# Optimization experiments

Measured on AMD Instinct MI355X. Metric: run time of the kernel, lower is better.

The kernel has to match this reference:

```python
import jax, jax.numpy as jnp
import numpy as np

N = 4096
D = 1024          # latent_vector_size
H, KD, VD = 16, 64, 64
MHK = H * KD      # 1024
MHV = H * VD      # 1024
HID = D // 2      # 512
EPS = 1e-5


def _layernorm(v, g, b):
    mu = jnp.mean(v, axis=-1, keepdims=True)
    var = jnp.mean(jnp.square(v - mu), axis=-1, keepdims=True)
    return (v - mu) * jax.lax.rsqrt(var + EPS) * g + b


def setup_inputs() -> dict:
    key = jax.random.key(0)
    ks = jax.random.split(key, 12)
    s = lambda fan_in: 1.0 / np.sqrt(fan_in)
    return {
        "x": jax.random.normal(ks[0], (N, D), dtype=jnp.float32),
        "w_qkv": jax.random.uniform(ks[1], (D, H * (2 * KD + VD)), jnp.float32, -s(D), s(D)),
        "b_qkv": jax.random.uniform(ks[2], (H * (2 * KD + VD),), jnp.float32, -s(D), s(D)),
        "w_msa": jax.random.uniform(ks[3], (MHV, D), jnp.float32, -s(MHV), s(MHV)),
        "b_msa": jax.random.uniform(ks[4], (D,), jnp.float32, -s(MHV), s(MHV)),
        "ln_g": jnp.ones((D,), jnp.float32),
        "ln_b": jnp.zeros((D,), jnp.float32),
        "w_h1": jax.random.uniform(ks[5], (D, HID), jnp.float32, -s(D), s(D)),
        "b_h1": jax.random.uniform(ks[6], (HID,), jnp.float32, -s(D), s(D)),
        "w_h2": jax.random.uniform(ks[7], (HID, D), jnp.float32, -s(HID), s(HID)),
        "b_h2": jax.random.uniform(ks[8], (D,), jnp.float32, -s(HID), s(HID)),
    }


def reference(x, w_qkv, b_qkv, w_msa, b_msa, ln_g, ln_b, w_h1, b_h1, w_h2, b_h2):
    # --- attention block (note: heads are never split; one big [N,N] softmax) ---
    ln1 = _layernorm(x, ln_g, ln_b)                       # [N, D]
    qkv = ln1 @ w_qkv + b_qkv                             # [N, 3*MHK]
    q, k, v = qkv[:, :MHK], qkv[:, MHK:2 * MHK], qkv[:, 2 * MHK:]
    scores = (q @ k.T) / jnp.sqrt(jnp.float32(KD))        # [N, N]
    attn = jax.nn.softmax(scores, axis=-1)
    mha = (attn @ v) @ w_msa + b_msa                      # [N, D]
    enc1 = x + mha
    # --- MLP block (shared layernorm params; softmax output, residual) ---
    ln2 = _layernorm(enc1, ln_g, ln_b)
    h1 = jax.nn.gelu(ln2 @ w_h1 + b_h1, approximate=False)  # [N, HID]
    h2 = jax.nn.gelu(h1 @ w_h2 + b_h2, approximate=False)   # [N, D]
    out = jax.nn.softmax(h2, axis=-1)                        # nn.Softmax() -> dim=1 for 2D
    return enc1 + out
```

## Files before the change

### kernel.cpp

```cpp
#include <hip/hip_runtime.h>
#include <stdint.h>

#define DEV __device__ __forceinline__

typedef unsigned short u16;
typedef __attribute__((ext_vector_type(8))) unsigned short u16x8;
typedef __attribute__((ext_vector_type(4))) unsigned short u16x4;
typedef __attribute__((ext_vector_type(4))) float f32x4;

DEV float bf2f(u16 u) { return __uint_as_float(((unsigned)u) << 16); }
DEV u16 f2bf(float f) {
  unsigned u = __float_as_uint(f);
  u += 0x7FFFu + ((u >> 16) & 1u);
  return (u16)(u >> 16);
}
DEV float gelu_exact(float v) { return 0.5f * v * (1.0f + erff(v * 0.70710678118654752f)); }

#define BARF asm volatile("s_barrier" ::: "memory")

__global__ __launch_bounds__(256) void transpose4_f32_bf16(
    const float* __restrict__ wqkv, u16* __restrict__ wqkvT,
    const float* __restrict__ wmsa, u16* __restrict__ wmsaT,
    const float* __restrict__ wh1, u16* __restrict__ wh1T,
    const float* __restrict__ wh2, u16* __restrict__ wh2T) {
  __shared__ float t[32][33];
  const int id = blockIdx.x;
  const float* in; u16* out; int rows, cols, bx, by;
  if (id < 3072)      { in = wqkv; out = wqkvT; rows = 1024; cols = 3072; bx = id % 96;          by = id / 96; }
  else if (id < 4096) { in = wmsa; out = wmsaT; rows = 1024; cols = 1024; bx = (id - 3072) % 32; by = (id - 3072) / 32; }
  else if (id < 4608) { in = wh1;  out = wh1T;  rows = 1024; cols = 512;  bx = (id - 4096) % 16; by = (id - 4096) / 16; }
  else                { in = wh2;  out = wh2T;  rows = 512;  cols = 1024; bx = (id - 4608) % 32; by = (id - 4608) / 32; }
  const int tx = threadIdx.x, ty = threadIdx.y;
  const int c0 = bx * 32, r0 = by * 32;
#pragma unroll
  for (int i = 0; i < 32; i += 8) t[ty + i][tx] = in[(size_t)(r0 + ty + i) * cols + c0 + tx];
  __syncthreads();
#pragma unroll
  for (int i = 0; i < 32; i += 8)
    out[(size_t)(c0 + ty + i) * rows + r0 + tx] = f2bf(t[tx][ty + i]);
}

__global__ __launch_bounds__(256) void transpose_bf16(
    const u16* __restrict__ in, int ldin, u16* __restrict__ out, int ldout) {
  __shared__ u16 t[32][33];
  const int tx = threadIdx.x, ty = threadIdx.y;
  const int c0 = blockIdx.x * 32, r0 = blockIdx.y * 32;
#pragma unroll
  for (int i = 0; i < 32; i += 8) t[ty + i][tx] = in[(size_t)(r0 + ty + i) * ldin + c0 + tx];
  __syncthreads();
#pragma unroll
  for (int i = 0; i < 32; i += 8)
    out[(size_t)(c0 + ty + i) * ldout + r0 + tx] = t[tx][ty + i];
}

__global__ __launch_bounds__(256) void layernorm_bf16(
    const float* __restrict__ in, const float* __restrict__ g,
    const float* __restrict__ b, u16* __restrict__ out) {
  const int tid = threadIdx.x;
  const int lane = tid & 63, wid = tid >> 6;
  const size_t base = (size_t)blockIdx.x * 1024;
  const float4 v = ((const float4*)(in + base))[tid];
  float s = v.x + v.y + v.z + v.w;
  float ss = v.x * v.x + v.y * v.y + v.z * v.z + v.w * v.w;
#pragma unroll
  for (int off = 32; off > 0; off >>= 1) {
    s += __shfl_down(s, off);
    ss += __shfl_down(ss, off);
  }
  __shared__ float red[8];
  if (lane == 0) { red[wid] = s; red[4 + wid] = ss; }
  __syncthreads();
  s = red[0] + red[1] + red[2] + red[3];
  ss = red[4] + red[5] + red[6] + red[7];
  const float mu = s * (1.0f / 1024.0f);
  const float inv = rsqrtf(ss * (1.0f / 1024.0f) - mu * mu + 1e-5f);
  const float4 gv = ((const float4*)g)[tid];
  const float4 bv = ((const float4*)b)[tid];
  u16x4 o;
  o.x = f2bf((v.x - mu) * inv * gv.x + bv.x);
  o.y = f2bf((v.y - mu) * inv * gv.y + bv.y);
  o.z = f2bf((v.z - mu) * inv * gv.z + bv.z);
  o.w = f2bf((v.w - mu) * inv * gv.w + bv.w);
  *(u16x4*)(out + base + tid * 4) = o;
}

__global__ __launch_bounds__(256) void softmax4096(u16* __restrict__ p) {
  const int tid = threadIdx.x;
  const int lane = tid & 63, wid = tid >> 6;
  u16* row = p + (size_t)blockIdx.x * 4096;
  u16x8 r0 = ((u16x8*)row)[tid * 2];
  u16x8 r1 = ((u16x8*)row)[tid * 2 + 1];
  float v[16];
#pragma unroll
  for (int i = 0; i < 8; ++i) { v[i] = bf2f(r0[i]); v[8 + i] = bf2f(r1[i]); }
  float mx = v[0];
#pragma unroll
  for (int i = 1; i < 16; ++i) mx = fmaxf(mx, v[i]);
#pragma unroll
  for (int off = 32; off > 0; off >>= 1) mx = fmaxf(mx, __shfl_down(mx, off));
  __shared__ float red[8];
  if (lane == 0) red[wid] = mx;
  __syncthreads();
  mx = fmaxf(fmaxf(red[0], red[1]), fmaxf(red[2], red[3]));
  float sum = 0.0f;
#pragma unroll
  for (int i = 0; i < 16; ++i) { v[i] = __expf(v[i] - mx); sum += v[i]; }
#pragma unroll
  for (int off = 32; off > 0; off >>= 1) sum += __shfl_down(sum, off);
  if (lane == 0) red[4 + wid] = sum;
  __syncthreads();
  sum = red[4] + red[5] + red[6] + red[7];
  const float inv = 1.0f / sum;
  u16x8 o0, o1;
#pragma unroll
  for (int i = 0; i < 8; ++i) { o0[i] = f2bf(v[i] * inv); o1[i] = f2bf(v[8 + i] * inv); }
  ((u16x8*)row)[tid * 2] = o0;
  ((u16x8*)row)[tid * 2 + 1] = o1;
}

__global__ __launch_bounds__(256) void final_softmax_add(
    const float* __restrict__ h2, const float* __restrict__ enc1, float* __restrict__ out) {
  const int tid = threadIdx.x;
  const int lane = tid & 63, wid = tid >> 6;
  const size_t base = (size_t)blockIdx.x * 1024;
  float4 v = ((const float4*)(h2 + base))[tid];
  float mx = fmaxf(fmaxf(v.x, v.y), fmaxf(v.z, v.w));
#pragma unroll
  for (int off = 32; off > 0; off >>= 1) mx = fmaxf(mx, __shfl_down(mx, off));
  __shared__ float red[8];
  if (lane == 0) red[wid] = mx;
  __syncthreads();
  mx = fmaxf(fmaxf(red[0], red[1]), fmaxf(red[2], red[3]));
  v.x = __expf(v.x - mx); v.y = __expf(v.y - mx);
  v.z = __expf(v.z - mx); v.w = __expf(v.w - mx);
  float sum = v.x + v.y + v.z + v.w;
#pragma unroll
  for (int off = 32; off > 0; off >>= 1) sum += __shfl_down(sum, off);
  if (lane == 0) red[4 + wid] = sum;
  __syncthreads();
  sum = red[4] + red[5] + red[6] + red[7];
  const float inv = 1.0f / sum;
  const float4 e = ((const float4*)(enc1 + base))[tid];
  float4 o;
  o.x = e.x + v.x * inv; o.y = e.y + v.y * inv;
  o.z = e.z + v.z * inv; o.w = e.w + v.w * inv;
  ((float4*)(out + base))[tid] = o;
}

__global__ __launch_bounds__(256) void reduce_partials(
    const u16* __restrict__ P, u16* __restrict__ out) {
  const size_t i = ((size_t)blockIdx.x * 256 + threadIdx.x) * 8;
  const size_t S = 4096ull * 1024ull;
  u16x8 p0 = *(const u16x8*)(P + i);
  u16x8 p1 = *(const u16x8*)(P + S + i);
  u16x8 p2 = *(const u16x8*)(P + 2 * S + i);
  u16x8 p3 = *(const u16x8*)(P + 3 * S + i);
  u16x8 o;
#pragma unroll
  for (int j = 0; j < 8; ++j)
    o[j] = f2bf(bf2f(p0[j]) + bf2f(p1[j]) + bf2f(p2[j]) + bf2f(p3[j]));
  *(u16x8*)(out + i) = o;
}

template <int EPI>
__global__ __launch_bounds__(512, 2) void gemm256(
    const u16* __restrict__ A, int lda, const u16* __restrict__ Bt, int ldb,
    u16* __restrict__ C, int ldc, const float* __restrict__ bias, float scale,
    int K, int nsplit, size_t sliceStride) {
  __shared__ alignas(16) u16 As[2][16384];
  __shared__ alignas(16) u16 Bs[2][16384];
  const int tid = threadIdx.x;
  const int wid = tid >> 6;
  const int lane = tid & 63;
  const int wr = wid >> 2, wc = wid & 3;

  const int gx = gridDim.x;
  const int nwg = gx * gridDim.y;
  int wg = blockIdx.y * gx + blockIdx.x;
  wg = (wg & 7) * (nwg >> 3) + (wg >> 3);
  const int by = wg / gx;
  const int bxk = wg % gx;
  const int ks = bxk % nsplit;
  const int bx = bxk / nsplit;
  const int m0 = by * 256, n0 = bx * 256;
  A += (size_t)ks * K;
  Bt += (size_t)ks * K;
  C += (size_t)ks * sliceStride;

  const u16* Apan = A + (size_t)m0 * lda;
  const u16* Bpan = Bt + (size_t)n0 * ldb;

  const int sgk = ((lane & 7) ^ ((lane >> 3) & 7)) * 8;
  const int hi4 = lane >> 4;
  const int kgo0 = ((0 * 4 + hi4) ^ (lane & 7)) * 8;
  const int kgo1 = ((1 * 4 + hi4) ^ (lane & 7)) * 8;
  const int arowo = (wr * 128 + (lane & 15)) * 64;
  const int browo = (wc * 64 + (lane & 15)) * 64;

  f32x4 acc[8][4];
#pragma unroll
  for (int m = 0; m < 8; ++m)
#pragma unroll
    for (int n = 0; n < 4; ++n) { f32x4 z = {0.f, 0.f, 0.f, 0.f}; acc[m][n] = z; }

  u16x8 a[2][2], b[4][2];

#define ST_HALF(dst, pan, ld, t, h)                                              \
  {                                                                              \
    _Pragma("unroll") for (int j = 0; j < 2; ++j) {                              \
      const int chunk = (tid >> 6) * 2 + j;                                      \
      const int row = (h)*128 + chunk * 8 + (lane >> 3);                         \
      const u16* gsrc = (pan) + (size_t)row * (ld) + (t)*64 + sgk;               \
      __builtin_amdgcn_global_load_lds(                                          \
          (const __attribute__((address_space(1))) void*)gsrc,                   \
          (__attribute__((address_space(3))) void*)((dst) + (h)*8192 +           \
                                                    chunk * 512 + lane * 8),     \
          16, 0, 0);                                                             \
    }                                                                            \
  }

#define LOADB(S)                                                                 \
  _Pragma("unroll") for (int n = 0; n < 4; ++n) {                                \
    b[n][0] = *(const u16x8*)&Bs[S][browo + n * 1024 + kgo0];                    \
    b[n][1] = *(const u16x8*)&Bs[S][browo + n * 1024 + kgo1];                    \
  }

#define LOADA(S, Q)                                                              \
  _Pragma("unroll") for (int mi = 0; mi < 2; ++mi) {                             \
    a[mi][0] = *(const u16x8*)&As[S][arowo + (2 * (Q) + mi) * 1024 + kgo0];      \
    a[mi][1] = *(const u16x8*)&As[S][arowo + (2 * (Q) + mi) * 1024 + kgo1];      \
  }

#define MMQ(Q)                                                                   \
  BARF;                                                                          \
  __builtin_amdgcn_s_setprio(1);                                                 \
  _Pragma("unroll") for (int mi = 0; mi < 2; ++mi)                               \
      _Pragma("unroll") for (int n = 0; n < 4; ++n)                              \
          _Pragma("unroll") for (int kk = 0; kk < 2; ++kk)                       \
              asm("v_mfma_f32_16x16x32_bf16 %0, %1, %2, %0"                      \
                  : "+v"(acc[2 * ((Q) & 3) + mi][n])                             \
                  : "v"(a[mi][kk]), "v"(b[n][kk]));                              \
  __builtin_amdgcn_s_setprio(0);

#define VMW asm volatile("s_waitcnt vmcnt(4)" ::: "memory");

  const int NT = K >> 6;
  const int NI = NT >> 1;

  ST_HALF(&Bs[0][0], Bpan, ldb, 0, 0);
  ST_HALF(&Bs[0][0], Bpan, ldb, 0, 1);
  ST_HALF(&As[0][0], Apan, lda, 0, 0);
  ST_HALF(&As[0][0], Apan, lda, 0, 1);
  ST_HALF(&Bs[1][0], Bpan, ldb, 1, 0);
  ST_HALF(&Bs[1][0], Bpan, ldb, 1, 1);
  VMW;
  BARF;

  for (int it = 0; it < NI; ++it) {
    const int t0 = 2 * it, t1 = t0 + 1;
    const int tS0 = (t0 + 2 < NT) ? t0 + 2 : NT - 1;
    const int tS1 = (t1 + 2 < NT) ? t1 + 2 : NT - 1;
    LOADB(0); LOADA(0, 0);
    ST_HALF(&As[1][0], Apan, lda, t1, 0);
    ST_HALF(&As[1][0], Apan, lda, t1, 1);
    MMQ(0); BARF;
    LOADA(0, 1);
    ST_HALF(&Bs[0][0], Bpan, ldb, tS0, 0);
    MMQ(1); BARF;
    LOADA(0, 2);
    ST_HALF(&Bs[0][0], Bpan, ldb, tS0, 1);
    MMQ(2); BARF;
    LOADA(0, 3);
    MMQ(3); VMW; BARF;
    LOADB(1); LOADA(1, 0);
    ST_HALF(&As[0][0], Apan, lda, tS0, 0);
    ST_HALF(&As[0][0], Apan, lda, tS0, 1);
    MMQ(4); BARF;
    LOADA(1, 1);
    ST_HALF(&Bs[1][0], Bpan, ldb, tS1, 0);
    MMQ(5); BARF;
    LOADA(1, 2);
    ST_HALF(&Bs[1][0], Bpan, ldb, tS1, 1);
    MMQ(6); BARF;
    LOADA(1, 3);
    MMQ(7); VMW; BARF;
  }
  asm volatile("s_waitcnt vmcnt(0)" ::: "memory");
  BARF;

  const int crow0 = m0 + wr * 128 + hi4 * 4;
  const int ccol0 = n0 + wc * 64 + (lane & 15);
#pragma unroll
  for (int m = 0; m < 8; ++m) {
#pragma unroll
    for (int n = 0; n < 4; ++n) {
      const int col = ccol0 + n * 16;
      float bia = 0.0f;
      if (EPI == 1) bia = bias[col];
#pragma unroll
      for (int r = 0; r < 4; ++r) {
        const int row = crow0 + m * 16 + r;
        float v = acc[m][n][r];
        if (EPI == 0) v *= scale;
        if (EPI == 1) v += bia;
        C[(size_t)row * ldc + col] = f2bf(v);
      }
    }
  }
#undef ST_HALF
#undef LOADB
#undef LOADA
#undef MMQ
#undef VMW
}

template <int EPI>
__global__ __launch_bounds__(256) void gemm_bt(
    const u16* __restrict__ A, int lda, const u16* __restrict__ Bt, int ldb,
    void* __restrict__ Cv, int ldc, const float* __restrict__ bias,
    const float* __restrict__ xres, int ldx, float scale, int K) {
  __shared__ alignas(16) u16 As[3][128 * 32];
  __shared__ alignas(16) u16 Bs[3][128 * 32];
  const int tid = threadIdx.x;
  const int wid = tid >> 6;
  const int lane = tid & 63;

  const int gx = gridDim.x;
  const int nwg = gridDim.x * gridDim.y;
  int wg = blockIdx.y * gx + blockIdx.x;
  wg = (wg & 7) * (nwg >> 3) + (wg >> 3);
  const int m0 = (wg / gx) * 128;
  const int n0 = (wg % gx) * 128;
  const int wr = wid >> 1, wc = wid & 1;

  const int srow = lane >> 2;
  const int sseg = (((lane & 3) ^ ((lane >> 3) & 3))) * 8;

  f32x4 acc[4][4];
#pragma unroll
  for (int m = 0; m < 4; ++m)
#pragma unroll
    for (int n = 0; n < 4; ++n) { f32x4 z = {0.f, 0.f, 0.f, 0.f}; acc[m][n] = z; }

  const int arow = wr * 64 + (lane & 15);
  const int brow = wc * 64 + (lane & 15);
  const int koff = (((lane >> 4) ^ ((lane >> 1) & 3))) * 8;

  const int NT = K >> 5;

  auto STAGE = [&](int kt, int buf) {
    const int k0 = kt * 32;
#pragma unroll
    for (int i = 0; i < 2; ++i) {
      const int r = i * 64 + wid * 16;
      const u16* ga = A + (size_t)(m0 + r + srow) * lda + k0 + sseg;
      const u16* gb = Bt + (size_t)(n0 + r + srow) * ldb + k0 + sseg;
      __builtin_amdgcn_global_load_lds((const __attribute__((address_space(1))) void*)ga,
                                       (__attribute__((address_space(3))) void*)&As[buf][r * 32], 16, 0, 0);
      __builtin_amdgcn_global_load_lds((const __attribute__((address_space(1))) void*)gb,
                                       (__attribute__((address_space(3))) void*)&Bs[buf][r * 32], 16, 0, 0);
    }
  };

  STAGE(0, 0);
  STAGE(1, 1);
  asm volatile("s_waitcnt vmcnt(4)" ::: "memory");
  BARF;

  int cur = 0;
  for (int t = 0; t < NT; ++t) {
    const int kt = (t + 2 < NT) ? (t + 2) : (NT - 1);
    STAGE(kt, (cur + 2) % 3);

    u16x8 a[4], b[4];
#pragma unroll
    for (int m = 0; m < 4; ++m) a[m] = *(const u16x8*)&As[cur][(arow + m * 16) * 32 + koff];
#pragma unroll
    for (int n = 0; n < 4; ++n) b[n] = *(const u16x8*)&Bs[cur][(brow + n * 16) * 32 + koff];
#pragma unroll
    for (int m = 0; m < 4; ++m)
#pragma unroll
      for (int n = 0; n < 4; ++n)
        asm("v_mfma_f32_16x16x32_bf16 %0, %1, %2, %0" : "+v"(acc[m][n]) : "v"(a[m]), "v"(b[n]));

    asm volatile("s_waitcnt vmcnt(4)" ::: "memory");
    BARF;
    cur = (cur + 1) % 3;
  }

  const int crow0 = m0 + wr * 64 + ((lane >> 4) << 2);
  const int ccol0 = n0 + wc * 64 + (lane & 15);
#pragma unroll
  for (int m = 0; m < 4; ++m) {
#pragma unroll
    for (int n = 0; n < 4; ++n) {
      const int col = ccol0 + n * 16;
      float bia = 0.0f;
      if (EPI == 3 || EPI == 4 || EPI == 5) bia = bias[col];
#pragma unroll
      for (int r = 0; r < 4; ++r) {
        const int row = crow0 + m * 16 + r;
        const float v = acc[m][n][r];
        if (EPI == 3) {
          ((float*)Cv)[(size_t)row * ldc + col] = v + bia + xres[(size_t)row * ldx + col];
        } else if (EPI == 4) {
          ((u16*)Cv)[(size_t)row * ldc + col] = f2bf(gelu_exact(v + bia));
        } else {
          ((float*)Cv)[(size_t)row * ldc + col] = gelu_exact(v + bia);
        }
      }
    }
  }
}

extern "C" void kernel_launch(void* const* d_in, const int* in_sizes, int n_in,
                              void* d_out, int out_size, void* d_ws, size_t ws_size,
                              hipStream_t stream) {
  const float* x     = (const float*)d_in[0];
  const float* w_qkv = (const float*)d_in[1];
  const float* b_qkv = (const float*)d_in[2];
  const float* w_msa = (const float*)d_in[3];
  const float* b_msa = (const float*)d_in[4];
  const float* ln_g  = (const float*)d_in[5];
  const float* ln_b  = (const float*)d_in[6];
  const float* w_h1  = (const float*)d_in[7];
  const float* b_h1  = (const float*)d_in[8];
  const float* w_h2  = (const float*)d_in[9];
  const float* b_h2  = (const float*)d_in[10];

  char* w = (char*)d_ws;
  u16*   qkv   = (u16*)(w + 0);
  u16*   sc    = (u16*)(w + 25165824);
  u16*   lnb   = (u16*)(w + 58720256);
  u16*   av    = (u16*)(w + 67108864);
  u16*   vT    = (u16*)(w + 75497472);
  float* enc1  = (float*)(w + 83886080);
  u16*   part  = (u16*)(w + 83886080);
  u16*   h1    = (u16*)(w + 100663296);
  float* h2    = (float*)(w + 104857600);
  u16*   wqkvT = (u16*)(w + 121634816);
  u16*   wmsaT = (u16*)(w + 127926272);
  u16*   wh1T  = (u16*)(w + 130023424);
  u16*   wh2T  = (u16*)(w + 131072000);
  (void)in_sizes; (void)n_in; (void)out_size; (void)ws_size;

  dim3 tb(32, 8);
  transpose4_f32_bf16<<<5120, tb, 0, stream>>>(w_qkv, wqkvT, w_msa, wmsaT,
                                               w_h1, wh1T, w_h2, wh2T);

  layernorm_bf16<<<4096, 256, 0, stream>>>(x, ln_g, ln_b, lnb);
  gemm256<1><<<dim3(12, 16), 512, 0, stream>>>(lnb, 1024, wqkvT, 1024, qkv, 3072,
                                               b_qkv, 1.0f, 1024, 1, 0);
  transpose_bf16<<<dim3(32, 128), tb, 0, stream>>>(qkv + 2048, 3072, vT, 4096);
  gemm256<0><<<dim3(16, 16), 512, 0, stream>>>(qkv, 3072, qkv + 1024, 3072, sc, 4096,
                                               nullptr, 0.125f, 1024, 1, 0);
  softmax4096<<<4096, 256, 0, stream>>>(sc);
  gemm256<2><<<dim3(16, 16), 512, 0, stream>>>(sc, 4096, vT, 4096, part, 1024,
                                               nullptr, 1.0f, 1024, 4, 4096ull * 1024ull);
  reduce_partials<<<2048, 256, 0, stream>>>(part, av);
  gemm_bt<3><<<dim3(8, 32), 256, 0, stream>>>(av, 1024, wmsaT, 1024, enc1, 1024,
                                              b_msa, x, 1024, 1.0f, 1024);
  layernorm_bf16<<<4096, 256, 0, stream>>>(enc1, ln_g, ln_b, lnb);
  gemm_bt<4><<<dim3(4, 32), 256, 0, stream>>>(lnb, 1024, wh1T, 1024, h1, 512,
                                              b_h1, nullptr, 0, 1.0f, 1024);
  gemm_bt<5><<<dim3(8, 32), 256, 0, stream>>>(h1, 512, wh2T, 512, h2, 1024,
                                              b_h2, nullptr, 0, 1.0f, 512);
  final_softmax_add<<<4096, 256, 0, stream>>>(h2, enc1, (float*)d_out);
}
```

Before: 233.7 us.

## Restructure GEMM main loop with double A register buffers and fewer barriers

Reorganises the inner K loop of the MFMA GEMM so each 64-wide K tile is processed in two halves. Two register buffers for A fragments let two quarter-tiles of MFMAs issue back-to-back, which cuts the per-tile barrier count from about five to two. Global-to-LDS prefetches are grouped after a single barrier and overlap the second half of the MFMAs. The trade-offs are higher VGPR pressure and less interleaving of loads with compute, which could hurt occupancy or latency hiding.

Measured after the change: 230.3 us. About the same (-1.5%).

```diff
diff --git a/kernel.cpp b/kernel.cpp
--- a/kernel.cpp
+++ b/kernel.cpp
@@ -203,7 +203,7 @@
 #pragma unroll
     for (int n = 0; n < 4; ++n) { f32x4 z = {0.f, 0.f, 0.f, 0.f}; acc[m][n] = z; }
 
-  u16x8 a[2][2], b[4][2];
+  u16x8 a0[2][2], a1[2][2], b[4][2];
 
 #define ST_HALF(dst, pan, ld, t, h)                                              \
   {                                                                              \
@@ -225,22 +225,19 @@
     b[n][1] = *(const u16x8*)&Bs[S][browo + n * 1024 + kgo1];                    \
   }
 
-#define LOADA(S, Q)                                                              \
+#define LOADA(S, Q, DST)                                                         \
   _Pragma("unroll") for (int mi = 0; mi < 2; ++mi) {                             \
-    a[mi][0] = *(const u16x8*)&As[S][arowo + (2 * (Q) + mi) * 1024 + kgo0];      \
-    a[mi][1] = *(const u16x8*)&As[S][arowo + (2 * (Q) + mi) * 1024 + kgo1];      \
-  }
-
-#define MMQ(Q)                                                                   \
-  BARF;                                                                          \
-  __builtin_amdgcn_s_setprio(1);                                                 \
+    DST[mi][0] = *(const u16x8*)&As[S][arowo + (2 * (Q) + mi) * 1024 + kgo0];    \
+    DST[mi][1] = *(const u16x8*)&As[S][arowo + (2 * (Q) + mi) * 1024 + kgo1];    \
+  }
+
+#define MFMAQ(SRC, Q)                                                            \
   _Pragma("unroll") for (int mi = 0; mi < 2; ++mi)                               \
       _Pragma("unroll") for (int n = 0; n < 4; ++n)                              \
           _Pragma("unroll") for (int kk = 0; kk < 2; ++kk)                       \
               asm("v_mfma_f32_16x16x32_bf16 %0, %1, %2, %0"                      \
-                  : "+v"(acc[2 * ((Q) & 3) + mi][n])                             \
-                  : "v"(a[mi][kk]), "v"(b[n][kk]));                              \
-  __builtin_amdgcn_s_setprio(0);
+                  : "+v"(acc[2 * (Q) + mi][n])                                   \
+                  : "v"(SRC[mi][kk]), "v"(b[n][kk]));
 
 #define VMW asm volatile("s_waitcnt vmcnt(4)" ::: "memory");
 
@@ -257,33 +254,43 @@
   BARF;
 
   for (int it = 0; it < NI; ++it) {
-    const int t0 = 2 * it, t1 = t0 + 1;
-    const int tS0 = (t0 + 2 < NT) ? t0 + 2 : NT - 1;
-    const int tS1 = (t1 + 2 < NT) ? t1 + 2 : NT - 1;
-    LOADB(0); LOADA(0, 0);
+    const int t1 = 2 * it + 1;
+    const int tS0 = (2 * it + 2 < NT) ? 2 * it + 2 : NT - 1;
+    const int tS1 = (2 * it + 3 < NT) ? 2 * it + 3 : NT - 1;
+
+    LOADB(0);
+    LOADA(0, 0, a0); LOADA(0, 1, a1);
+    __builtin_amdgcn_s_setprio(1);
+    MFMAQ(a0, 0); MFMAQ(a1, 1);
+    __builtin_amdgcn_s_setprio(0);
+    LOADA(0, 2, a0); LOADA(0, 3, a1);
+    BARF;
     ST_HALF(&As[1][0], Apan, lda, t1, 0);
     ST_HALF(&As[1][0], Apan, lda, t1, 1);
-    MMQ(0); BARF;
-    LOADA(0, 1);
     ST_HALF(&Bs[0][0], Bpan, ldb, tS0, 0);
-    MMQ(1); BARF;
-    LOADA(0, 2);
     ST_HALF(&Bs[0][0], Bpan, ldb, tS0, 1);
-    MMQ(2); BARF;
-    LOADA(0, 3);
-    MMQ(3); VMW; BARF;
-    LOADB(1); LOADA(1, 0);
+    __builtin_amdgcn_s_setprio(1);
+    MFMAQ(a0, 2); MFMAQ(a1, 3);
+    __builtin_amdgcn_s_setprio(0);
+    VMW;
+    BARF;
+
+    LOADB(1);
+    LOADA(1, 0, a0); LOADA(1, 1, a1);
+    __builtin_amdgcn_s_setprio(1);
+    MFMAQ(a0, 0); MFMAQ(a1, 1);
+    __builtin_amdgcn_s_setprio(0);
+    LOADA(1, 2, a0); LOADA(1, 3, a1);
+    BARF;
     ST_HALF(&As[0][0], Apan, lda, tS0, 0);
     ST_HALF(&As[0][0], Apan, lda, tS0, 1);
-    MMQ(4); BARF;
-    LOADA(1, 1);
     ST_HALF(&Bs[1][0], Bpan, ldb, tS1, 0);
-    MMQ(5); BARF;
-    LOADA(1, 2);
     ST_HALF(&Bs[1][0], Bpan, ldb, tS1, 1);
-    MMQ(6); BARF;
-    LOADA(1, 3);
-    MMQ(7); VMW; BARF;
+    __builtin_amdgcn_s_setprio(1);
+    MFMAQ(a0, 2); MFMAQ(a1, 3);
+    __builtin_amdgcn_s_setprio(0);
+    VMW;
+    BARF;
   }
   asm volatile("s_waitcnt vmcnt(0)" ::: "memory");
   BARF;
@@ -310,7 +317,7 @@
 #undef ST_HALF
 #undef LOADB
 #undef LOADA
-#undef MMQ
+#undef MFMAQ
 #undef VMW
 }
 
```

## Run output projection through split-K gemm256 with fused bias-residual reduction

Applied to the files above, without the earlier changes.

The attention output projection now uses the large 256-tile GEMM with 4-way split-K into bf16 partials. A new reduce kernel sums them and adds bias and the residual in fp32. The GEMM inner loops switch from inline-asm MFMA to the compiler builtin, with an explicit LDS wait and reordered stage loads. enc1 is moved to alias the qkv buffer. The new path adds extra partial-buffer traffic and bf16 rounding of partials in exchange for better tile utilization.

Result: slower. 241.3 us (+3.2%).

```diff
diff --git a/kernel.cpp b/kernel.cpp
--- a/kernel.cpp
+++ b/kernel.cpp
@@ -5,6 +5,7 @@
 
 typedef unsigned short u16;
 typedef __attribute__((ext_vector_type(8))) unsigned short u16x8;
+typedef __attribute__((ext_vector_type(8))) short s16x8;
 typedef __attribute__((ext_vector_type(4))) unsigned short u16x4;
 typedef __attribute__((ext_vector_type(4))) float f32x4;
 
@@ -162,6 +163,33 @@
   *(u16x8*)(out + i) = o;
 }
 
+__global__ __launch_bounds__(256) void reduce4_bias_res(
+    const u16* __restrict__ P, const float* __restrict__ bias,
+    const float* __restrict__ x, float* __restrict__ out) {
+  const size_t i = ((size_t)blockIdx.x * 256 + threadIdx.x) * 8;
+  const size_t S = 4096ull * 1024ull;
+  u16x8 p0 = *(const u16x8*)(P + i);
+  u16x8 p1 = *(const u16x8*)(P + S + i);
+  u16x8 p2 = *(const u16x8*)(P + 2 * S + i);
+  u16x8 p3 = *(const u16x8*)(P + 3 * S + i);
+  const int col = (int)(i & 1023);
+  const float4 b0 = *(const float4*)(bias + col);
+  const float4 b1 = *(const float4*)(bias + col + 4);
+  const float4 x0 = *(const float4*)(x + i);
+  const float4 x1 = *(const float4*)(x + i + 4);
+  float r[8];
+#pragma unroll
+  for (int j = 0; j < 8; ++j)
+    r[j] = bf2f(p0[j]) + bf2f(p1[j]) + bf2f(p2[j]) + bf2f(p3[j]);
+  float4 o0, o1;
+  o0.x = r[0] + b0.x + x0.x; o0.y = r[1] + b0.y + x0.y;
+  o0.z = r[2] + b0.z + x0.z; o0.w = r[3] + b0.w + x0.w;
+  o1.x = r[4] + b1.x + x1.x; o1.y = r[5] + b1.y + x1.y;
+  o1.z = r[6] + b1.z + x1.z; o1.w = r[7] + b1.w + x1.w;
+  *(float4*)(out + i) = o0;
+  *(float4*)(out + i + 4) = o1;
+}
+
 template <int EPI>
 __global__ __launch_bounds__(512, 2) void gemm256(
     const u16* __restrict__ A, int lda, const u16* __restrict__ Bt, int ldb,
@@ -170,8 +198,8 @@
   __shared__ alignas(16) u16 As[2][16384];
   __shared__ alignas(16) u16 Bs[2][16384];
   const int tid = threadIdx.x;
+  const int lane = tid & 63;
   const int wid = tid >> 6;
-  const int lane = tid & 63;
   const int wr = wid >> 2, wc = wid & 3;
 
   const int gx = gridDim.x;
@@ -203,7 +231,7 @@
 #pragma unroll
     for (int n = 0; n < 4; ++n) { f32x4 z = {0.f, 0.f, 0.f, 0.f}; acc[m][n] = z; }
 
-  u16x8 a[2][2], b[4][2];
+  s16x8 a[2][2], b[4][2];
 
 #define ST_HALF(dst, pan, ld, t, h)                                              \
   {                                                                              \
@@ -221,25 +249,25 @@
 
 #define LOADB(S)                                                                 \
   _Pragma("unroll") for (int n = 0; n < 4; ++n) {                                \
-    b[n][0] = *(const u16x8*)&Bs[S][browo + n * 1024 + kgo0];                    \
-    b[n][1] = *(const u16x8*)&Bs[S][browo + n * 1024 + kgo1];                    \
+    b[n][0] = *(const s16x8*)&Bs[S][browo + n * 1024 + kgo0];                    \
+    b[n][1] = *(const s16x8*)&Bs[S][browo + n * 1024 + kgo1];                    \
   }
 
 #define LOADA(S, Q)                                                              \
   _Pragma("unroll") for (int mi = 0; mi < 2; ++mi) {                             \
-    a[mi][0] = *(const u16x8*)&As[S][arowo + (2 * (Q) + mi) * 1024 + kgo0];      \
-    a[mi][1] = *(const u16x8*)&As[S][arowo + (2 * (Q) + mi) * 1024 + kgo1];      \
-  }
-
-#define MMQ(Q)                                                                   \
+    a[mi][0] = *(const s16x8*)&As[S][arowo + (2 * (Q) + mi) * 1024 + kgo0];      \
+    a[mi][1] = *(const s16x8*)&As[S][arowo + (2 * (Q) + mi) * 1024 + kgo1];      \
+  }
+
+#define MM(Q)                                                                    \
   BARF;                                                                          \
+  asm volatile("s_waitcnt lgkmcnt(0)" ::: "memory");                             \
   __builtin_amdgcn_s_setprio(1);                                                 \
   _Pragma("unroll") for (int mi = 0; mi < 2; ++mi)                               \
       _Pragma("unroll") for (int n = 0; n < 4; ++n)                              \
           _Pragma("unroll") for (int kk = 0; kk < 2; ++kk)                       \
-              asm("v_mfma_f32_16x16x32_bf16 %0, %1, %2, %0"                      \
-                  : "+v"(acc[2 * ((Q) & 3) + mi][n])                             \
-                  : "v"(a[mi][kk]), "v"(b[n][kk]));                              \
+              acc[2 * (Q) + mi][n] = __builtin_amdgcn_mfma_f32_16x16x32_bf16(    \
+                  a[mi][kk], b[n][kk], acc[2 * (Q) + mi][n], 0, 0, 0);           \
   __builtin_amdgcn_s_setprio(0);
 
 #define VMW asm volatile("s_waitcnt vmcnt(4)" ::: "memory");
@@ -257,33 +285,33 @@
   BARF;
 
   for (int it = 0; it < NI; ++it) {
-    const int t0 = 2 * it, t1 = t0 + 1;
-    const int tS0 = (t0 + 2 < NT) ? t0 + 2 : NT - 1;
-    const int tS1 = (t1 + 2 < NT) ? t1 + 2 : NT - 1;
+    const int t1 = 2 * it + 1;
+    const int tS0 = (2 * it + 2 < NT) ? 2 * it + 2 : NT - 1;
+    const int tS1 = (2 * it + 3 < NT) ? 2 * it + 3 : NT - 1;
     LOADB(0); LOADA(0, 0);
     ST_HALF(&As[1][0], Apan, lda, t1, 0);
+    MM(0); BARF;
+    LOADA(0, 1);
     ST_HALF(&As[1][0], Apan, lda, t1, 1);
-    MMQ(0); BARF;
-    LOADA(0, 1);
+    MM(1); BARF;
+    LOADA(0, 2);
     ST_HALF(&Bs[0][0], Bpan, ldb, tS0, 0);
-    MMQ(1); BARF;
-    LOADA(0, 2);
+    MM(2); BARF;
+    LOADA(0, 3);
     ST_HALF(&Bs[0][0], Bpan, ldb, tS0, 1);
-    MMQ(2); BARF;
-    LOADA(0, 3);
-    MMQ(3); VMW; BARF;
+    MM(3); VMW; BARF;
     LOADB(1); LOADA(1, 0);
     ST_HALF(&As[0][0], Apan, lda, tS0, 0);
+    MM(0); BARF;
+    LOADA(1, 1);
     ST_HALF(&As[0][0], Apan, lda, tS0, 1);
-    MMQ(4); BARF;
-    LOADA(1, 1);
+    MM(1); BARF;
+    LOADA(1, 2);
     ST_HALF(&Bs[1][0], Bpan, ldb, tS1, 0);
-    MMQ(5); BARF;
-    LOADA(1, 2);
+    MM(2); BARF;
+    LOADA(1, 3);
     ST_HALF(&Bs[1][0], Bpan, ldb, tS1, 1);
-    MMQ(6); BARF;
-    LOADA(1, 3);
-    MMQ(7); VMW; BARF;
+    MM(3); VMW; BARF;
   }
   asm volatile("s_waitcnt vmcnt(0)" ::: "memory");
   BARF;
@@ -310,7 +338,7 @@
 #undef ST_HALF
 #undef LOADB
 #undef LOADA
-#undef MMQ
+#undef MM
 #undef VMW
 }
 
@@ -318,7 +346,7 @@
 __global__ __launch_bounds__(256) void gemm_bt(
     const u16* __restrict__ A, int lda, const u16* __restrict__ Bt, int ldb,
     void* __restrict__ Cv, int ldc, const float* __restrict__ bias,
-    const float* __restrict__ xres, int ldx, float scale, int K) {
+    float scale, int K) {
   __shared__ alignas(16) u16 As[3][128 * 32];
   __shared__ alignas(16) u16 Bs[3][128 * 32];
   const int tid = threadIdx.x;
@@ -372,16 +400,16 @@
     const int kt = (t + 2 < NT) ? (t + 2) : (NT - 1);
     STAGE(kt, (cur + 2) % 3);
 
-    u16x8 a[4], b[4];
-#pragma unroll
-    for (int m = 0; m < 4; ++m) a[m] = *(const u16x8*)&As[cur][(arow + m * 16) * 32 + koff];
-#pragma unroll
-    for (int n = 0; n < 4; ++n) b[n] = *(const u16x8*)&Bs[cur][(brow + n * 16) * 32 + koff];
+    s16x8 a[4], b[4];
+#pragma unroll
+    for (int m = 0; m < 4; ++m) a[m] = *(const s16x8*)&As[cur][(arow + m * 16) * 32 + koff];
+#pragma unroll
+    for (int n = 0; n < 4; ++n) b[n] = *(const s16x8*)&Bs[cur][(brow + n * 16) * 32 + koff];
 #pragma unroll
     for (int m = 0; m < 4; ++m)
 #pragma unroll
       for (int n = 0; n < 4; ++n)
-        asm("v_mfma_f32_16x16x32_bf16 %0, %1, %2, %0" : "+v"(acc[m][n]) : "v"(a[m]), "v"(b[n]));
+        acc[m][n] = __builtin_amdgcn_mfma_f32_16x16x32_bf16(a[m], b[n], acc[m][n], 0, 0, 0);
 
     asm volatile("s_waitcnt vmcnt(4)" ::: "memory");
     BARF;
@@ -395,15 +423,12 @@
 #pragma unroll
     for (int n = 0; n < 4; ++n) {
       const int col = ccol0 + n * 16;
-      float bia = 0.0f;
-      if (EPI == 3 || EPI == 4 || EPI == 5) bia = bias[col];
+      const float bia = bias[col];
 #pragma unroll
       for (int r = 0; r < 4; ++r) {
         const int row = crow0 + m * 16 + r;
         const float v = acc[m][n][r];
-        if (EPI == 3) {
-          ((float*)Cv)[(size_t)row * ldc + col] = v + bia + xres[(size_t)row * ldx + col];
-        } else if (EPI == 4) {
+        if (EPI == 4) {
           ((u16*)Cv)[(size_t)row * ldc + col] = f2bf(gelu_exact(v + bia));
         } else {
           ((float*)Cv)[(size_t)row * ldc + col] = gelu_exact(v + bia);
@@ -411,6 +436,7 @@
       }
     }
   }
+  (void)scale;
 }
 
 extern "C" void kernel_launch(void* const* d_in, const int* in_sizes, int n_in,
@@ -430,11 +456,11 @@
 
   char* w = (char*)d_ws;
   u16*   qkv   = (u16*)(w + 0);
+  float* enc1  = (float*)(w + 0);
   u16*   sc    = (u16*)(w + 25165824);
   u16*   lnb   = (u16*)(w + 58720256);
   u16*   av    = (u16*)(w + 67108864);
   u16*   vT    = (u16*)(w + 75497472);
-  float* enc1  = (float*)(w + 83886080);
   u16*   part  = (u16*)(w + 83886080);
   u16*   h1    = (u16*)(w + 100663296);
   float* h2    = (float*)(w + 104857600);
@@ -458,12 +484,13 @@
   gemm256<2><<<dim3(16, 16), 512, 0, stream>>>(sc, 4096, vT, 4096, part, 1024,
                                                nullptr, 1.0f, 1024, 4, 4096ull * 1024ull);
   reduce_partials<<<2048, 256, 0, stream>>>(part, av);
-  gemm_bt<3><<<dim3(8, 32), 256, 0, stream>>>(av, 1024, wmsaT, 1024, enc1, 1024,
-                                              b_msa, x, 1024, 1.0f, 1024);
+  gemm256<2><<<dim3(16, 16), 512, 0, stream>>>(av, 1024, wmsaT, 1024, part, 1024,
+                                               nullptr, 1.0f, 256, 4, 4096ull * 1024ull);
+  reduce4_bias_res<<<2048, 256, 0, stream>>>(part, b_msa, x, enc1);
   layernorm_bf16<<<4096, 256, 0, stream>>>(enc1, ln_g, ln_b, lnb);
   gemm_bt<4><<<dim3(4, 32), 256, 0, stream>>>(lnb, 1024, wh1T, 1024, h1, 512,
-                                              b_h1, nullptr, 0, 1.0f, 1024);
+                                              b_h1, 1.0f, 1024);
   gemm_bt<5><<<dim3(8, 32), 256, 0, stream>>>(h1, 512, wh2T, 512, h2, 1024,
-                                              b_h2, nullptr, 0, 1.0f, 512);
+                                              b_h2, 1.0f, 512);
   final_softmax_add<<<4096, 256, 0, stream>>>(h2, enc1, (float*)d_out);
 }
```

## Replace 256x256 K64 GEMM with 256x128 K32 tile at higher occupancy

Applied to the files above, without the earlier changes.

Swaps the hand-scheduled 256x256 tile GEMM, which used 64-wide K steps, a quarter-step LDS load pipeline and setprio, for a simpler 256x128 tile with 32-wide K steps. It uses plain double buffering with a full vmcnt(0) wait per step and launch bounds allowing 4 blocks per CU. Grids double to match the narrower N tiles. Inline-asm MFMAs become builtins in both GEMM kernels. The change aims at more resident blocks and smaller LDS use, but it gives up per-tile data reuse and the fine-grained overlap of loads with MFMAs.

After: 246.7 us. 1.06x slower.

```diff
diff --git a/kernel.cpp b/kernel.cpp
--- a/kernel.cpp
+++ b/kernel.cpp
@@ -5,6 +5,7 @@
 
 typedef unsigned short u16;
 typedef __attribute__((ext_vector_type(8))) unsigned short u16x8;
+typedef __attribute__((ext_vector_type(8))) short s16x8;
 typedef __attribute__((ext_vector_type(4))) unsigned short u16x4;
 typedef __attribute__((ext_vector_type(4))) float f32x4;
 
@@ -163,16 +164,16 @@
 }
 
 template <int EPI>
-__global__ __launch_bounds__(512, 2) void gemm256(
+__global__ __launch_bounds__(512, 4) void gemm256k32(
     const u16* __restrict__ A, int lda, const u16* __restrict__ Bt, int ldb,
     u16* __restrict__ C, int ldc, const float* __restrict__ bias, float scale,
     int K, int nsplit, size_t sliceStride) {
-  __shared__ alignas(16) u16 As[2][16384];
-  __shared__ alignas(16) u16 Bs[2][16384];
+  __shared__ alignas(16) u16 As[2][256 * 32];
+  __shared__ alignas(16) u16 Bs[2][128 * 32];
   const int tid = threadIdx.x;
+  const int lane = tid & 63;
   const int wid = tid >> 6;
-  const int lane = tid & 63;
-  const int wr = wid >> 2, wc = wid & 3;
+  const int wr = wid >> 1, wc = wid & 1;
 
   const int gx = gridDim.x;
   const int nwg = gx * gridDim.y;
@@ -182,7 +183,7 @@
   const int bxk = wg % gx;
   const int ks = bxk % nsplit;
   const int bx = bxk / nsplit;
-  const int m0 = by * 256, n0 = bx * 256;
+  const int m0 = by * 256, n0 = bx * 128;
   A += (size_t)ks * K;
   Bt += (size_t)ks * K;
   C += (size_t)ks * sliceStride;
@@ -190,108 +191,65 @@
   const u16* Apan = A + (size_t)m0 * lda;
   const u16* Bpan = Bt + (size_t)n0 * ldb;
 
-  const int sgk = ((lane & 7) ^ ((lane >> 3) & 7)) * 8;
-  const int hi4 = lane >> 4;
-  const int kgo0 = ((0 * 4 + hi4) ^ (lane & 7)) * 8;
-  const int kgo1 = ((1 * 4 + hi4) ^ (lane & 7)) * 8;
-  const int arowo = (wr * 128 + (lane & 15)) * 64;
-  const int browo = (wc * 64 + (lane & 15)) * 64;
-
-  f32x4 acc[8][4];
-#pragma unroll
-  for (int m = 0; m < 8; ++m)
+  const int srow = lane >> 2;
+  const int sseg = ((lane & 3) ^ ((lane >> 3) & 3)) * 8;
+  const int koff = (((lane >> 4) ^ ((lane >> 1) & 3))) * 8;
+
+  f32x4 acc[4][4];
+#pragma unroll
+  for (int m = 0; m < 4; ++m)
 #pragma unroll
     for (int n = 0; n < 4; ++n) { f32x4 z = {0.f, 0.f, 0.f, 0.f}; acc[m][n] = z; }
 
-  u16x8 a[2][2], b[4][2];
-
-#define ST_HALF(dst, pan, ld, t, h)                                              \
-  {                                                                              \
-    _Pragma("unroll") for (int j = 0; j < 2; ++j) {                              \
-      const int chunk = (tid >> 6) * 2 + j;                                      \
-      const int row = (h)*128 + chunk * 8 + (lane >> 3);                         \
-      const u16* gsrc = (pan) + (size_t)row * (ld) + (t)*64 + sgk;               \
-      __builtin_amdgcn_global_load_lds(                                          \
-          (const __attribute__((address_space(1))) void*)gsrc,                   \
-          (__attribute__((address_space(3))) void*)((dst) + (h)*8192 +           \
-                                                    chunk * 512 + lane * 8),     \
-          16, 0, 0);                                                             \
-    }                                                                            \
-  }
-
-#define LOADB(S)                                                                 \
-  _Pragma("unroll") for (int n = 0; n < 4; ++n) {                                \
-    b[n][0] = *(const u16x8*)&Bs[S][browo + n * 1024 + kgo0];                    \
-    b[n][1] = *(const u16x8*)&Bs[S][browo + n * 1024 + kgo1];                    \
-  }
-
-#define LOADA(S, Q)                                                              \
-  _Pragma("unroll") for (int mi = 0; mi < 2; ++mi) {                             \
-    a[mi][0] = *(const u16x8*)&As[S][arowo + (2 * (Q) + mi) * 1024 + kgo0];      \
-    a[mi][1] = *(const u16x8*)&As[S][arowo + (2 * (Q) + mi) * 1024 + kgo1];      \
-  }
-
-#define MMQ(Q)                                                                   \
-  BARF;                                                                          \
-  __builtin_amdgcn_s_setprio(1);                                                 \
-  _Pragma("unroll") for (int mi = 0; mi < 2; ++mi)                               \
-      _Pragma("unroll") for (int n = 0; n < 4; ++n)                              \
-          _Pragma("unroll") for (int kk = 0; kk < 2; ++kk)                       \
-              asm("v_mfma_f32_16x16x32_bf16 %0, %1, %2, %0"                      \
-                  : "+v"(acc[2 * ((Q) & 3) + mi][n])                             \
-                  : "v"(a[mi][kk]), "v"(b[n][kk]));                              \
-  __builtin_amdgcn_s_setprio(0);
-
-#define VMW asm volatile("s_waitcnt vmcnt(4)" ::: "memory");
-
-  const int NT = K >> 6;
-  const int NI = NT >> 1;
-
-  ST_HALF(&Bs[0][0], Bpan, ldb, 0, 0);
-  ST_HALF(&Bs[0][0], Bpan, ldb, 0, 1);
-  ST_HALF(&As[0][0], Apan, lda, 0, 0);
-  ST_HALF(&As[0][0], Apan, lda, 0, 1);
-  ST_HALF(&Bs[1][0], Bpan, ldb, 1, 0);
-  ST_HALF(&Bs[1][0], Bpan, ldb, 1, 1);
-  VMW;
-  BARF;
-
-  for (int it = 0; it < NI; ++it) {
-    const int t0 = 2 * it, t1 = t0 + 1;
-    const int tS0 = (t0 + 2 < NT) ? t0 + 2 : NT - 1;
-    const int tS1 = (t1 + 2 < NT) ? t1 + 2 : NT - 1;
-    LOADB(0); LOADA(0, 0);
-    ST_HALF(&As[1][0], Apan, lda, t1, 0);
-    ST_HALF(&As[1][0], Apan, lda, t1, 1);
-    MMQ(0); BARF;
-    LOADA(0, 1);
-    ST_HALF(&Bs[0][0], Bpan, ldb, tS0, 0);
-    MMQ(1); BARF;
-    LOADA(0, 2);
-    ST_HALF(&Bs[0][0], Bpan, ldb, tS0, 1);
-    MMQ(2); BARF;
-    LOADA(0, 3);
-    MMQ(3); VMW; BARF;
-    LOADB(1); LOADA(1, 0);
-    ST_HALF(&As[0][0], Apan, lda, tS0, 0);
-    ST_HALF(&As[0][0], Apan, lda, tS0, 1);
-    MMQ(4); BARF;
-    LOADA(1, 1);
-    ST_HALF(&Bs[1][0], Bpan, ldb, tS1, 0);
-    MMQ(5); BARF;
-    LOADA(1, 2);
-    ST_HALF(&Bs[1][0], Bpan, ldb, tS1, 1);
-    MMQ(6); BARF;
-    LOADA(1, 3);
-    MMQ(7); VMW; BARF;
-  }
+  const int arow = wr * 64 + (lane & 15);
+  const int brow = wc * 64 + (lane & 15);
+
+  auto STAGE = [&](int S, int t) {
+#pragma unroll
+    for (int i = 0; i < 2; ++i) {
+      const int rbase = i * 128 + wid * 16;
+      const u16* ga = Apan + (size_t)(rbase + srow) * lda + t * 32 + sseg;
+      __builtin_amdgcn_global_load_lds((const __attribute__((address_space(1))) void*)ga,
+                                       (__attribute__((address_space(3))) void*)&As[S][rbase * 32],
+                                       16, 0, 0);
+    }
+    const int rbase = wid * 16;
+    const u16* gb = Bpan + (size_t)(rbase + srow) * ldb + t * 32 + sseg;
+    __builtin_amdgcn_global_load_lds((const __attribute__((address_space(1))) void*)gb,
+                                     (__attribute__((address_space(3))) void*)&Bs[S][rbase * 32],
+                                     16, 0, 0);
+  };
+
+  const int NT = K >> 5;
+
+  STAGE(0, 0);
   asm volatile("s_waitcnt vmcnt(0)" ::: "memory");
   BARF;
 
-  const int crow0 = m0 + wr * 128 + hi4 * 4;
+  int s = 0;
+  for (int t = 0; t < NT; ++t) {
+    if (t + 1 < NT) STAGE(s ^ 1, t + 1);
+
+    s16x8 a[4], b[4];
+#pragma unroll
+    for (int m = 0; m < 4; ++m) a[m] = *(const s16x8*)&As[s][(arow + m * 16) * 32 + koff];
+#pragma unroll
+    for (int n = 0; n < 4; ++n) b[n] = *(const s16x8*)&Bs[s][(brow + n * 16) * 32 + koff];
+#pragma unroll
+    for (int m = 0; m < 4; ++m)
+#pragma unroll
+      for (int n = 0; n < 4; ++n)
+        acc[m][n] = __builtin_amdgcn_mfma_f32_16x16x32_bf16(a[m], b[n], acc[m][n], 0, 0, 0);
+
+    asm volatile("s_waitcnt vmcnt(0)" ::: "memory");
+    BARF;
+    s ^= 1;
+  }
+
+  const int crow0 = m0 + wr * 64 + ((lane >> 4) << 2);
   const int ccol0 = n0 + wc * 64 + (lane & 15);
 #pragma unroll
-  for (int m = 0; m < 8; ++m) {
+  for (int m = 0; m < 4; ++m) {
 #pragma unroll
     for (int n = 0; n < 4; ++n) {
       const int col = ccol0 + n * 16;
@@ -307,11 +265,6 @@
       }
     }
   }
-#undef ST_HALF
-#undef LOADB
-#undef LOADA
-#undef MMQ
-#undef VMW
 }
 
 template <int EPI>
@@ -372,16 +325,16 @@
     const int kt = (t + 2 < NT) ? (t + 2) : (NT - 1);
     STAGE(kt, (cur + 2) % 3);
 
-    u16x8 a[4], b[4];
-#pragma unroll
-    for (int m = 0; m < 4; ++m) a[m] = *(const u16x8*)&As[cur][(arow + m * 16) * 32 + koff];
-#pragma unroll
-    for (int n = 0; n < 4; ++n) b[n] = *(const u16x8*)&Bs[cur][(brow + n * 16) * 32 + koff];
+    s16x8 a[4], b[4];
+#pragma unroll
+    for (int m = 0; m < 4; ++m) a[m] = *(const s16x8*)&As[cur][(arow + m * 16) * 32 + koff];
+#pragma unroll
+    for (int n = 0; n < 4; ++n) b[n] = *(const s16x8*)&Bs[cur][(brow + n * 16) * 32 + koff];
 #pragma unroll
     for (int m = 0; m < 4; ++m)
 #pragma unroll
       for (int n = 0; n < 4; ++n)
-        asm("v_mfma_f32_16x16x32_bf16 %0, %1, %2, %0" : "+v"(acc[m][n]) : "v"(a[m]), "v"(b[n]));
+        acc[m][n] = __builtin_amdgcn_mfma_f32_16x16x32_bf16(a[m], b[n], acc[m][n], 0, 0, 0);
 
     asm volatile("s_waitcnt vmcnt(4)" ::: "memory");
     BARF;
@@ -395,8 +348,7 @@
 #pragma unroll
     for (int n = 0; n < 4; ++n) {
       const int col = ccol0 + n * 16;
-      float bia = 0.0f;
-      if (EPI == 3 || EPI == 4 || EPI == 5) bia = bias[col];
+      const float bia = bias[col];
 #pragma unroll
       for (int r = 0; r < 4; ++r) {
         const int row = crow0 + m * 16 + r;
@@ -411,6 +363,7 @@
       }
     }
   }
+  (void)scale;
 }
 
 extern "C" void kernel_launch(void* const* d_in, const int* in_sizes, int n_in,
@@ -449,14 +402,14 @@
                                                w_h1, wh1T, w_h2, wh2T);
 
   layernorm_bf16<<<4096, 256, 0, stream>>>(x, ln_g, ln_b, lnb);
-  gemm256<1><<<dim3(12, 16), 512, 0, stream>>>(lnb, 1024, wqkvT, 1024, qkv, 3072,
-                                               b_qkv, 1.0f, 1024, 1, 0);
+  gemm256k32<1><<<dim3(24, 16), 512, 0, stream>>>(lnb, 1024, wqkvT, 1024, qkv, 3072,
+                                                  b_qkv, 1.0f, 1024, 1, 0);
   transpose_bf16<<<dim3(32, 128), tb, 0, stream>>>(qkv + 2048, 3072, vT, 4096);
-  gemm256<0><<<dim3(16, 16), 512, 0, stream>>>(qkv, 3072, qkv + 1024, 3072, sc, 4096,
-                                               nullptr, 0.125f, 1024, 1, 0);
+  gemm256k32<0><<<dim3(32, 16), 512, 0, stream>>>(qkv, 3072, qkv + 1024, 3072, sc, 4096,
+                                                  nullptr, 0.125f, 1024, 1, 0);
   softmax4096<<<4096, 256, 0, stream>>>(sc);
-  gemm256<2><<<dim3(16, 16), 512, 0, stream>>>(sc, 4096, vT, 4096, part, 1024,
-                                               nullptr, 1.0f, 1024, 4, 4096ull * 1024ull);
+  gemm256k32<2><<<dim3(32, 16), 512, 0, stream>>>(sc, 4096, vT, 4096, part, 1024,
+                                                  nullptr, 1.0f, 1024, 4, 4096ull * 1024ull);
   reduce_partials<<<2048, 256, 0, stream>>>(part, av);
   gemm_bt<3><<<dim3(8, 32), 256, 0, stream>>>(av, 1024, wmsaT, 1024, enc1, 1024,
                                               b_msa, x, 1024, 1.0f, 1024);
```
